# Performance work log

Hardware: AMD Instinct MI355X
Metric: run time of the kernel (lower is better)

## Reference

```python
import jax, jax.numpy as jnp
import numpy as np

DEPTH = 10
N_LEAF = 1024        # = n_nodes = 2**DEPTH
FEATURE_LENGTH = 1024
BATCH = 16384


def setup_inputs() -> dict:
    key = jax.random.key(0)
    kx, kidx, kw, kb = jax.random.split(key, 4)
    x = jax.random.normal(kx, (BATCH, FEATURE_LENGTH), dtype=jnp.float32)
    # feature_mask: one-hot column selection, onehot[using_idx].T -> [feature_length, n_leaf]
    using_idx = jax.random.randint(kidx, (N_LEAF,), 0, FEATURE_LENGTH)
    feature_mask = jax.nn.one_hot(using_idx, FEATURE_LENGTH, dtype=jnp.float32).T
    # n_nodes tiny Linear(n_leaf, 1) layers batched into one [n_leaf, n_nodes] weight
    W = jax.random.normal(kw, (N_LEAF, N_LEAF), dtype=jnp.float32) / np.sqrt(N_LEAF)
    b = jax.random.normal(kb, (N_LEAF,), dtype=jnp.float32) * 0.01
    return {"x": x, "feature_mask": feature_mask, "W": W, "b": b}


def reference(x, feature_mask, W, b):
    B = x.shape[0]
    feats = x @ feature_mask                      # [B, n_leaf]
    d = jax.nn.sigmoid(feats @ W + b)             # [B, n_nodes] (all node linears as one GEMM)
    decision = jnp.stack([d, 1.0 - d], axis=-1)   # [B, n_nodes, 2]
    mu = jnp.ones((B, 1), dtype=x.dtype)
    parts = [jnp.ones((B, 2), dtype=x.dtype)]     # initial big_mu of ones
    begin = 1                                     # node 0 is unused, matching original indexing
    for n_layer in range(DEPTH):
        n = 2 ** n_layer
        nd = decision[:, begin:begin + n, :]      # [B, n, 2]
        mu = (mu[:, :, None] * nd).reshape(B, 2 * n)
        parts.append(mu)
        begin += n
    return jnp.concatenate(parts, axis=1)         # [B, 2 + (2**(DEPTH+1) - 2)] = [B, 2048]
```

## Files before the change

### kernel.cpp

```cpp
#include <hip/hip_runtime.h>


typedef __bf16 bf16x8 __attribute__((ext_vector_type(8)));
typedef float  f32x4  __attribute__((ext_vector_type(4)));

#define BATCH 16384
#define NLEAF 1024
#define FEAT  1024
#define OUTC  2048

__device__ __forceinline__ unsigned short f2bf(float f) {
    union { float f; unsigned int u; } c; c.f = f;
    unsigned int u = c.u;
    u += 0x7FFFu + ((u >> 16) & 1u);
    return (unsigned short)(u >> 16);
}

__device__ __forceinline__ float bf2f(unsigned short u) {
    union { unsigned int i; float f; } c; c.i = (unsigned int)u << 16;
    return c.f;
}

__device__ __forceinline__ void load_lds16(const void* g, void* l) {
    __builtin_amdgcn_global_load_lds(
        (const __attribute__((address_space(1))) unsigned int*)g,
        (__attribute__((address_space(3))) unsigned int*)l, 16, 0, 0);
}

__device__ __forceinline__ float sigmoidf(float z) {
    return 1.0f / (1.0f + __expf(-z));
}

__global__ __launch_bounds__(256) void prep_w(const float* __restrict__ fm,
                                              const float* __restrict__ W,
                                              int* __restrict__ idx,
                                              short* __restrict__ Wt) {
    __shared__ short tile[64][65];
    const int b = blockIdx.x, t = threadIdx.x;
    if (b < 1024) {
        const int f = b;
#pragma unroll
        for (int i = 0; i < 4; ++i) {
            int leaf = i * 256 + t;
            if (fm[(size_t)f * NLEAF + leaf] > 0.5f) idx[leaf] = f;
        }
    } else {
        const int tb = b - 1024;
        const int k0 = (tb >> 4) * 64, n0 = (tb & 15) * 64;
#pragma unroll
        for (int i = 0; i < 16; ++i) {
            int e = i * 256 + t;
            int kr = e >> 6, nc = e & 63;
            tile[kr][nc] = (short)f2bf(W[(size_t)(k0 + kr) * NLEAF + n0 + nc]);
        }
        __syncthreads();
#pragma unroll
        for (int i = 0; i < 16; ++i) {
            int e = i * 256 + t;
            int nr = e >> 6, kc = e & 63;
            Wt[(size_t)(n0 + nr) * FEAT + k0 + kc] = tile[kc][nr];
        }
    }
}

__global__ __launch_bounds__(256) void gather_feats(const float* __restrict__ x,
                                                    const int* __restrict__ idx,
                                                    short* __restrict__ feats) {
    __shared__ float xs[8][1024];
    __shared__ int   ids[1024];
    const int t = threadIdx.x;
    const int r0 = blockIdx.x * 8;

    {
        int4 v = ((const int4*)idx)[t];
        *(int4*)&ids[t * 4] = v;
    }
#pragma unroll
    for (int j = 0; j < 8; ++j) {
        int e = j * 256 + t;
        int row = e >> 8, c4 = e & 255;
        ((float4*)xs[row])[c4] =
            ((const float4*)(x + (size_t)(r0 + row) * FEAT))[c4];
    }
    __syncthreads();

#pragma unroll
    for (int j = 0; j < 4; ++j) {
        int e = j * 256 + t;
        int row = e >> 7, kk = (e & 127) * 8;
        union { short s[8]; int4 v; } pk;
#pragma unroll
        for (int q = 0; q < 8; ++q)
            pk.s[q] = (short)f2bf(xs[row][ids[kk + q]]);
        *(int4*)(feats + (size_t)(r0 + row) * FEAT + kk) = pk.v;
    }
}

__global__ __launch_bounds__(256, 4) void gemm_sig_d(
        const short* __restrict__ feats, const short* __restrict__ Wt,
        const float* __restrict__ bias, unsigned short* __restrict__ dout) {
    __shared__ __align__(16) short As[2][128 * 32];
    __shared__ __align__(16) short Bs[2][128 * 32];

    const int t = threadIdx.x, l = t & 63, w = t >> 6;
    const int wr = w >> 1, wc = w & 1;
    const int lr = l & 15, lk = l >> 4;
    const int bid = blockIdx.x;
    const int swz = (bid & 7) * 128 + (bid >> 3);
    const int row0 = (swz >> 3) << 7;
    const int n0   = (swz & 7) << 7;

    float bvreg[4];
#pragma unroll
    for (int n = 0; n < 4; ++n) bvreg[n] = bias[n0 + wc * 64 + n * 16 + lr];

    int aoff[4], boff[4];
#pragma unroll
    for (int m = 0; m < 4; ++m) {
        int r = wr * 64 + m * 16 + lr;
        aoff[m] = r * 64 + ((lk ^ ((r ^ (r >> 2)) & 3)) << 4);
    }
#pragma unroll
    for (int n = 0; n < 4; ++n) {
        int r = wc * 64 + n * 16 + lr;
        boff[n] = r * 64 + ((lk ^ ((r ^ (r >> 2)) & 3)) << 4);
    }

    auto stage = [&](int ch, int buf) {
#pragma unroll
        for (int j = 0; j < 2; ++j) {
            int si = j * 256 + t;
            int row = si >> 2, ps = si & 3;
            int ss = ps ^ ((row ^ (row >> 2)) & 3);
            load_lds16(feats + (size_t)(row0 + row) * FEAT + (ch << 5) + (ss << 3),
                       &As[buf][si * 8]);
            load_lds16(Wt + (size_t)(n0 + row) * FEAT + (ch << 5) + (ss << 3),
                       &Bs[buf][si * 8]);
        }
    };

    f32x4 acc[4][4];
#pragma unroll
    for (int m = 0; m < 4; ++m)
#pragma unroll
        for (int n = 0; n < 4; ++n)
#pragma unroll
            for (int r = 0; r < 4; ++r) acc[m][n][r] = 0.0f;

    stage(0, 0);
    __syncthreads();

#define COMPUTE(BUF)                                                        \
    {                                                                       \
        bf16x8 av[4], bv[4];                                                \
        _Pragma("unroll")                                                   \
        for (int m = 0; m < 4; ++m)                                         \
            av[m] = *(const bf16x8*)((const char*)As[BUF] + aoff[m]);       \
        _Pragma("unroll")                                                   \
        for (int n = 0; n < 4; ++n)                                         \
            bv[n] = *(const bf16x8*)((const char*)Bs[BUF] + boff[n]);       \
        _Pragma("unroll")                                                   \
        for (int m = 0; m < 4; ++m)                                         \
            _Pragma("unroll")                                               \
            for (int n = 0; n < 4; ++n)                                     \
                acc[m][n] = __builtin_amdgcn_mfma_f32_16x16x32_bf16(        \
                    av[m], bv[n], acc[m][n], 0, 0, 0);                      \
    }

    for (int ch2 = 0; ch2 < 16; ++ch2) {
        {
            const int ch = ch2 * 2;
            if (ch < 31) stage(ch + 1, 1);
            COMPUTE(0);
            __syncthreads();
        }
        {
            const int ch = ch2 * 2 + 1;
            if (ch < 31) stage(ch + 1, 0);
            COMPUTE(1);
            __syncthreads();
        }
    }
#undef COMPUTE

#pragma unroll
    for (int m = 0; m < 4; ++m) {
#pragma unroll
        for (int n = 0; n < 4; ++n) {
            const int col = n0 + wc * 64 + n * 16 + lr;
#pragma unroll
            for (int rr = 0; rr < 4; ++rr) {
                const int row = row0 + wr * 64 + m * 16 + lk * 4 + rr;
                dout[(size_t)row * 4096 + 3072 + col] =
                    f2bf(sigmoidf(acc[m][n][rr] + bvreg[n]));
            }
        }
    }
}

__global__ __launch_bounds__(256) void expand_tree(float* __restrict__ out) {
    const int t = threadIdx.x, l = t & 63, w = t >> 6;
    const int row = blockIdx.x * 4 + w;
    const unsigned short* dr =
        (const unsigned short*)out + (size_t)row * 4096 + 3072;
    float* orow = out + (size_t)row * OUTC;

    float dpath[6];
#pragma unroll
    for (int j = 0; j <= 5; ++j) {
        int idx = l >> (5 - j);
        dpath[j] = bf2f(dr[(1 << j) + (idx >> 1)]);
    }
    float d6 = bf2f(dr[64 + l]);
    unsigned int u7 = *(const unsigned int*)(dr + 128 + 2 * l);
    float d7[2] = { bf2f((unsigned short)(u7 & 0xffff)),
                    bf2f((unsigned short)(u7 >> 16)) };
    uint2 u8 = *(const uint2*)(dr + 256 + 4 * l);
    float d8[4] = { bf2f((unsigned short)(u8.x & 0xffff)),
                    bf2f((unsigned short)(u8.x >> 16)),
                    bf2f((unsigned short)(u8.y & 0xffff)),
                    bf2f((unsigned short)(u8.y >> 16)) };
    uint4 u9 = *(const uint4*)(dr + 512 + 8 * l);
    float d9[8] = { bf2f((unsigned short)(u9.x & 0xffff)),
                    bf2f((unsigned short)(u9.x >> 16)),
                    bf2f((unsigned short)(u9.y & 0xffff)),
                    bf2f((unsigned short)(u9.y >> 16)),
                    bf2f((unsigned short)(u9.z & 0xffff)),
                    bf2f((unsigned short)(u9.z >> 16)),
                    bf2f((unsigned short)(u9.w & 0xffff)),
                    bf2f((unsigned short)(u9.w >> 16)) };

    float p = 1.0f;
#pragma unroll
    for (int j = 0; j <= 5; ++j) {
        int idx = l >> (5 - j);
        p *= (idx & 1) ? (1.0f - dpath[j]) : dpath[j];
        if ((l & ((1 << (5 - j)) - 1)) == 0)
            orow[(2 << j) + idx] = p;
    }
    if (l < 2) orow[l] = 1.0f;

    float v6[2] = { p * d6, p * (1.0f - d6) };
    *(float2*)(orow + 128 + 2 * l) = make_float2(v6[0], v6[1]);

    float v7[4];
#pragma unroll
    for (int e = 0; e < 4; ++e)
        v7[e] = v6[e >> 1] * ((e & 1) ? (1.0f - d7[e >> 1]) : d7[e >> 1]);
    *(float4*)(orow + 256 + 4 * l) = make_float4(v7[0], v7[1], v7[2], v7[3]);

    float v8[8];
#pragma unroll
    for (int e = 0; e < 8; ++e)
        v8[e] = v7[e >> 1] * ((e & 1) ? (1.0f - d8[e >> 1]) : d8[e >> 1]);
    *(float4*)(orow + 512 + 8 * l)     = make_float4(v8[0], v8[1], v8[2], v8[3]);
    *(float4*)(orow + 512 + 8 * l + 4) = make_float4(v8[4], v8[5], v8[6], v8[7]);

    float v9[16];
#pragma unroll
    for (int e = 0; e < 16; ++e)
        v9[e] = v8[e >> 1] * ((e & 1) ? (1.0f - d9[e >> 1]) : d9[e >> 1]);
#pragma unroll
    for (int q = 0; q < 4; ++q)
        *(float4*)(orow + 1024 + 16 * l + 4 * q) =
            make_float4(v9[4*q], v9[4*q+1], v9[4*q+2], v9[4*q+3]);
}

template <bool HAS_IDX>
__global__ __launch_bounds__(256) void fused_naive(const float* __restrict__ x,
                                                   const float* __restrict__ fm,
                                                   const float* __restrict__ W,
                                                   const float* __restrict__ bias,
                                                   const int* __restrict__ idx,
                                                   float* __restrict__ out) {
    __shared__ float fx[1024];
    __shared__ float dsm[1024];
    __shared__ float tre[2048];
    __shared__ int   idl[1024];
    const int t = threadIdx.x;
    const int row = blockIdx.x;

    if (HAS_IDX) {
        for (int k = t; k < 1024; k += 256) idl[k] = idx[k];
    } else {
        for (int k = t; k < 1024; k += 256) {
            int found = 0;
            for (int f = 0; f < 1024; ++f)
                if (fm[(size_t)f * NLEAF + k] > 0.5f) found = f;
            idl[k] = found;
        }
    }
    __syncthreads();
    const float* xr = x + (size_t)row * FEAT;
    for (int k = t; k < 1024; k += 256) fx[k] = xr[idl[k]];
    __syncthreads();

    float a0 = 0.f, a1 = 0.f, a2 = 0.f, a3 = 0.f;
    for (int k = 0; k < 1024; ++k) {
        float f = fx[k];
        const float* wrp = W + (size_t)k * NLEAF + t;
        a0 = fmaf(f, wrp[0],   a0);
        a1 = fmaf(f, wrp[256], a1);
        a2 = fmaf(f, wrp[512], a2);
        a3 = fmaf(f, wrp[768], a3);
    }
    dsm[t]       = sigmoidf(a0 + bias[t]);
    dsm[t + 256] = sigmoidf(a1 + bias[t + 256]);
    dsm[t + 512] = sigmoidf(a2 + bias[t + 512]);
    dsm[t + 768] = sigmoidf(a3 + bias[t + 768]);
    if (t < 2) tre[t] = 1.0f;
    __syncthreads();

    for (int L = 0; L < 10; ++L) {
        int n = 2 << L;
        for (int k = t; k < n; k += 256) {
            int node = (1 << L) + (k >> 1);
            float dv = dsm[node];
            tre[n + k] = tre[node] * ((k & 1) ? (1.0f - dv) : dv);
        }
        __syncthreads();
    }
    float4* orow = (float4*)(out + (size_t)row * OUTC);
    const float4* ts = (const float4*)tre;
    for (int i = t; i < 512; i += 256) orow[i] = ts[i];
}

extern "C" void kernel_launch(void* const* d_in, const int* in_sizes, int n_in,
                              void* d_out, int out_size, void* d_ws, size_t ws_size,
                              hipStream_t stream) {
    const float* x    = (const float*)d_in[0];
    const float* fm   = (const float*)d_in[1];
    const float* W    = (const float*)d_in[2];
    const float* bias = (const float*)d_in[3];
    float* out = (float*)d_out;

    const size_t IDX_B   = 4096;
    const size_t WT_B    = (size_t)NLEAF * FEAT * 2;
    const size_t FEATS_B = (size_t)BATCH * FEAT * 2;
    const size_t need = IDX_B + WT_B + FEATS_B;

    if (ws_size >= need) {
        int*   idx   = (int*)d_ws;
        short* Wt    = (short*)((char*)d_ws + IDX_B);
        short* feats = (short*)((char*)d_ws + IDX_B + WT_B);

        prep_w<<<1280, 256, 0, stream>>>(fm, W, idx, Wt);
        gather_feats<<<BATCH / 8, 256, 0, stream>>>(x, idx, feats);
        gemm_sig_d<<<(BATCH / 128) * (NLEAF / 128), 256, 0, stream>>>(
            feats, Wt, bias, (unsigned short*)out);
        expand_tree<<<BATCH / 4, 256, 0, stream>>>(out);
    } else if (ws_size >= IDX_B) {
        int* idx = (int*)d_ws;
        prep_w<<<1280, 256, 0, stream>>>(fm, nullptr, idx, nullptr);
        fused_naive<true><<<BATCH, 256, 0, stream>>>(x, fm, W, bias, idx, out);
    } else {
        fused_naive<false><<<BATCH, 256, 0, stream>>>(x, fm, W, bias, nullptr, out);
    }
}
```

Measured before the change: 103.6 us.

## Replace 128x128 GEMM with 256x256-tile 8-wave kernel using phased pipelining

Replaces the bf16 GEMM+sigmoid kernel with a 512-thread block computing a 256x256 output tile over K-steps of 64, using 128KB of LDS with double buffering and an XOR swizzle. Each K-step is split into four phases that interleave LDS reads, async global-to-LDS staging of the next tile, and MFMA bursts at raised wave priority. The larger tile raises arithmetic intensity and cuts global traffic per FLOP. The cost is higher register and LDS pressure: 128KB of LDS per block means at most two blocks fit per CU, and only 256 blocks are launched.

```diff
diff --git a/kernel.cpp b/kernel.cpp
--- a/kernel.cpp
+++ b/kernel.cpp
@@ -96,101 +96,129 @@
     }
 }
 
-__global__ __launch_bounds__(256, 4) void gemm_sig_d(
+
+#define STAGEH(P, TT, BUFN)                                                   \
+    {                                                                         \
+        constexpr int hh = (P) & 1;                                           \
+        _Pragma("unroll")                                                     \
+        for (int j = 0; j < 2; ++j) {                                         \
+            const int r = j * 64 + r8;                                        \
+            if ((P) < 2) {                                                    \
+                load_lds16(feats + (size_t)(row0 + hh * 128 + r) * FEAT       \
+                               + ((TT) << 6) + (ss << 3),                     \
+                           smem + (BUFN) * 32768 + hh * 16384                 \
+                               + (j * 512 + tid) * 16);                       \
+            } else {                                                          \
+                load_lds16(Wt + (size_t)(n0 + hh * 128 + r) * FEAT            \
+                               + ((TT) << 6) + (ss << 3),                     \
+                           smem + 65536 + (BUFN) * 32768 + hh * 16384         \
+                               + (j * 512 + tid) * 16);                       \
+            }                                                                 \
+        }                                                                     \
+    }
+
+#define GPHASE(P, DO_STAGE, DO_WAITV)                                         \
+    {                                                                         \
+        constexpr int qm = (P) >> 1, qn = (P) & 1;                            \
+        bf16x8 av[4][2], bv[2][2];                                            \
+        _Pragma("unroll")                                                     \
+        for (int mm = 0; mm < 4; ++mm)                                        \
+            _Pragma("unroll")                                                 \
+            for (int kh = 0; kh < 2; ++kh)                                    \
+                av[mm][kh] = *(const bf16x8*)(smem + bufA                     \
+                               + aRow[qm * 4 + mm] + slotoff[kh]);            \
+        _Pragma("unroll")                                                     \
+        for (int nn = 0; nn < 2; ++nn)                                        \
+            _Pragma("unroll")                                                 \
+            for (int kh = 0; kh < 2; ++kh)                                    \
+                bv[nn][kh] = *(const bf16x8*)(smem + bufA                     \
+                               + bRow[qn * 2 + nn] + slotoff[kh]);            \
+        if (DO_STAGE) STAGEH(P, t + 1, bufN);                                 \
+        __builtin_amdgcn_s_barrier();                                         \
+        asm volatile("s_waitcnt lgkmcnt(0)" ::: "memory");                    \
+        __builtin_amdgcn_sched_barrier(0);                                    \
+        __builtin_amdgcn_s_setprio(1);                                        \
+        _Pragma("unroll")                                                     \
+        for (int mm = 0; mm < 4; ++mm)                                        \
+            _Pragma("unroll")                                                 \
+            for (int nn = 0; nn < 2; ++nn)                                    \
+                _Pragma("unroll")                                             \
+                for (int kh = 0; kh < 2; ++kh)                                \
+                    acc[qm * 4 + mm][qn * 2 + nn] =                           \
+                        __builtin_amdgcn_mfma_f32_16x16x32_bf16(              \
+                            av[mm][kh], bv[nn][kh],                           \
+                            acc[qm * 4 + mm][qn * 2 + nn], 0, 0, 0);          \
+        __builtin_amdgcn_s_setprio(0);                                        \
+        if (DO_WAITV) { asm volatile("s_waitcnt vmcnt(0)" ::: "memory"); }    \
+        __builtin_amdgcn_s_barrier();                                         \
+    }
+
+__global__ __launch_bounds__(512, 2) void gemm256_sig_d(
         const short* __restrict__ feats, const short* __restrict__ Wt,
         const float* __restrict__ bias, unsigned short* __restrict__ dout) {
-    __shared__ __align__(16) short As[2][128 * 32];
-    __shared__ __align__(16) short Bs[2][128 * 32];
-
-    const int t = threadIdx.x, l = t & 63, w = t >> 6;
-    const int wr = w >> 1, wc = w & 1;
+    __shared__ __align__(16) char smem_[131072];
+    char* smem = smem_;
+
+    const int tid = threadIdx.x, l = tid & 63, w = tid >> 6;
+    const int wr = w >> 2, wc = w & 3;
     const int lr = l & 15, lk = l >> 4;
     const int bid = blockIdx.x;
-    const int swz = (bid & 7) * 128 + (bid >> 3);
-    const int row0 = (swz >> 3) << 7;
-    const int n0   = (swz & 7) << 7;
+    const int swz = (bid & 7) * 32 + (bid >> 3);
+    const int row0 = (swz >> 2) << 8;
+    const int n0   = (swz & 3) << 8;
+
+    const int r8 = tid >> 3;
+    const int ss = (tid & 7) ^ (r8 & 7);
+
+    int aRow[8], bRow[4], slotoff[2];
+#pragma unroll
+    for (int m = 0; m < 8; ++m)
+        aRow[m] = wr * 16384 + (m * 16 + lr) * 128;
+#pragma unroll
+    for (int n = 0; n < 4; ++n)
+        bRow[n] = 65536 + (wc >> 1) * 16384 + ((wc & 1) * 64 + n * 16 + lr) * 128;
+#pragma unroll
+    for (int kh = 0; kh < 2; ++kh)
+        slotoff[kh] = ((kh * 4 + lk) ^ (lr & 7)) * 16;
 
     float bvreg[4];
 #pragma unroll
-    for (int n = 0; n < 4; ++n) bvreg[n] = bias[n0 + wc * 64 + n * 16 + lr];
-
-    int aoff[4], boff[4];
-#pragma unroll
-    for (int m = 0; m < 4; ++m) {
-        int r = wr * 64 + m * 16 + lr;
-        aoff[m] = r * 64 + ((lk ^ ((r ^ (r >> 2)) & 3)) << 4);
-    }
-#pragma unroll
-    for (int n = 0; n < 4; ++n) {
-        int r = wc * 64 + n * 16 + lr;
-        boff[n] = r * 64 + ((lk ^ ((r ^ (r >> 2)) & 3)) << 4);
-    }
-
-    auto stage = [&](int ch, int buf) {
-#pragma unroll
-        for (int j = 0; j < 2; ++j) {
-            int si = j * 256 + t;
-            int row = si >> 2, ps = si & 3;
-            int ss = ps ^ ((row ^ (row >> 2)) & 3);
-            load_lds16(feats + (size_t)(row0 + row) * FEAT + (ch << 5) + (ss << 3),
-                       &As[buf][si * 8]);
-            load_lds16(Wt + (size_t)(n0 + row) * FEAT + (ch << 5) + (ss << 3),
-                       &Bs[buf][si * 8]);
-        }
-    };
-
-    f32x4 acc[4][4];
-#pragma unroll
-    for (int m = 0; m < 4; ++m)
+    for (int n = 0; n < 4; ++n)
+        bvreg[n] = bias[n0 + wc * 64 + n * 16 + lr];
+
+    f32x4 acc[8][4];
+#pragma unroll
+    for (int m = 0; m < 8; ++m)
 #pragma unroll
         for (int n = 0; n < 4; ++n)
 #pragma unroll
             for (int r = 0; r < 4; ++r) acc[m][n][r] = 0.0f;
 
-    stage(0, 0);
-    __syncthreads();
-
-#define COMPUTE(BUF)                                                        \
-    {                                                                       \
-        bf16x8 av[4], bv[4];                                                \
-        _Pragma("unroll")                                                   \
-        for (int m = 0; m < 4; ++m)                                         \
-            av[m] = *(const bf16x8*)((const char*)As[BUF] + aoff[m]);       \
-        _Pragma("unroll")                                                   \
-        for (int n = 0; n < 4; ++n)                                         \
-            bv[n] = *(const bf16x8*)((const char*)Bs[BUF] + boff[n]);       \
-        _Pragma("unroll")                                                   \
-        for (int m = 0; m < 4; ++m)                                         \
-            _Pragma("unroll")                                               \
-            for (int n = 0; n < 4; ++n)                                     \
-                acc[m][n] = __builtin_amdgcn_mfma_f32_16x16x32_bf16(        \
-                    av[m], bv[n], acc[m][n], 0, 0, 0);                      \
-    }
-
-    for (int ch2 = 0; ch2 < 16; ++ch2) {
-        {
-            const int ch = ch2 * 2;
-            if (ch < 31) stage(ch + 1, 1);
-            COMPUTE(0);
-            __syncthreads();
-        }
-        {
-            const int ch = ch2 * 2 + 1;
-            if (ch < 31) stage(ch + 1, 0);
-            COMPUTE(1);
-            __syncthreads();
-        }
-    }
-#undef COMPUTE
-
-#pragma unroll
-    for (int m = 0; m < 4; ++m) {
+    STAGEH(0, 0, 0);
+    STAGEH(1, 0, 0);
+    STAGEH(2, 0, 0);
+    STAGEH(3, 0, 0);
+    asm volatile("s_waitcnt vmcnt(0)" ::: "memory");
+    __builtin_amdgcn_s_barrier();
+
+    for (int t = 0; t < 16; ++t) {
+        const int bufA = (t & 1) * 32768;
+        const int bufN = (t & 1) ^ 1;
+        const bool st = (t < 15);
+        GPHASE(0, st, false);
+        GPHASE(1, st, false);
+        GPHASE(2, st, false);
+        GPHASE(3, st, st);
+    }
+
+#pragma unroll
+    for (int m = 0; m < 8; ++m) {
 #pragma unroll
         for (int n = 0; n < 4; ++n) {
             const int col = n0 + wc * 64 + n * 16 + lr;
 #pragma unroll
             for (int rr = 0; rr < 4; ++rr) {
-                const int row = row0 + wr * 64 + m * 16 + lk * 4 + rr;
+                const int row = row0 + wr * 128 + m * 16 + lk * 4 + rr;
                 dout[(size_t)row * 4096 + 3072 + col] =
                     f2bf(sigmoidf(acc[m][n][rr] + bvreg[n]));
             }
@@ -346,7 +374,7 @@
 
         prep_w<<<1280, 256, 0, stream>>>(fm, W, idx, Wt);
         gather_feats<<<BATCH / 8, 256, 0, stream>>>(x, idx, feats);
-        gemm_sig_d<<<(BATCH / 128) * (NLEAF / 128), 256, 0, stream>>>(
+        gemm256_sig_d<<<(BATCH / 256) * (NLEAF / 256), 512, 0, stream>>>(
             feats, Wt, bias, (unsigned short*)out);
         expand_tree<<<BATCH / 4, 256, 0, stream>>>(out);
     } else if (ws_size >= IDX_B) {
```

Result: no change. 101.5 us (-1.9%).
